# Kernel optimization log

Measured on AMD Instinct MI355X. Metric: run time of the kernel, lower is better.

The kernel has to match this reference:

```python
import jax, jax.numpy as jnp
import numpy as np

NUM_NODES = 32768  # B*N = 16*2048
NUM_REL = 10
NUM_BASES = 4
D = 256
E = 524288


def _rgcn_layer(x, src, dst, rel, basis, comp, root, bias):
    """Basis-decomposed relational GCN layer with per-relation mean aggregation.
    x: [N, Din], basis: [NB, Din, Dout], comp: [R, NB], root: [Din, Dout], bias: [Dout].
    """
    n = x.shape[0]
    # project all nodes through each basis once: [N, NB, Dout]
    xb = jnp.einsum('ni,bio->nbo', x, basis)
    coeff = comp[rel]  # [E, NB] per-edge basis coefficients
    # mean normalization per (destination node, relation) pair
    seg = rel * n + dst  # combined segment id, [E]
    cnt = jax.ops.segment_sum(jnp.ones(rel.shape[0], x.dtype), seg,
                              num_segments=NUM_REL * n)
    inv = jnp.where(cnt > 0, 1.0 / cnt, 0.0)[seg]  # [E]
    # per-edge message: sum_b coeff[e,b] * xb[src_e, b, :] (loop over small NB)
    msg = jnp.zeros((rel.shape[0], basis.shape[2]), x.dtype)
    for b in range(basis.shape[0]):
        msg = msg + coeff[:, b:b + 1] * xb[src, b]
    msg = msg * inv[:, None]
    agg = jax.ops.segment_sum(msg, dst, num_segments=n)  # [N, Dout]
    return agg + x @ root + bias


def setup_inputs() -> dict:
    key = jax.random.key(0)
    ks = jax.random.split(key, 16)
    p = lambda k, shp: (jax.random.normal(k, shp, jnp.float32) * 0.05)
    inp = {
        'x': jax.random.normal(ks[0], (16, 2048, D), jnp.float32),
        't': jax.random.randint(ks[1], (16,), 0, 1000),
        'obj_cond': jax.random.randint(ks[2], (16, 2048), 0, 160),
        'edge_cond': jax.random.randint(ks[3], (2, E), 0, NUM_NODES),
        'relation_cond': jax.random.randint(ks[4], (E,), 0, NUM_REL),
        # layer 0: 256 -> 256 (hidden)
        'basis0': p(ks[5], (NUM_BASES, D, D)),
        'comp0': p(ks[6], (NUM_REL, NUM_BASES)),
        'root0': p(ks[7], (D, D)),
        'bias0': p(ks[8], (D,)),
        # layer 1: 256 -> 256 (output)
        'basis1': p(ks[9], (NUM_BASES, D, D)),
        'comp1': p(ks[10], (NUM_REL, NUM_BASES)),
        'root1': p(ks[11], (D, D)),
        'bias1': p(ks[12], (D,)),
    }
    return inp


def reference(x, t, obj_cond, edge_cond, relation_cond,
              basis0, comp0, root0, bias0, basis1, comp1, root1, bias1):
    B, N, Dm = x.shape
    h = x.reshape(B * N, Dm)
    src, dst = edge_cond[0], edge_cond[1]
    h = _rgcn_layer(h, src, dst, relation_cond, basis0, comp0, root0, bias0)
    h = jax.nn.relu(h)  # hidden-layer activation (dropout disabled at eval)
    h = _rgcn_layer(h, src, dst, relation_cond, basis1, comp1, root1, bias1)
    return h.reshape(B, N, Dm)
```

## Files before the change

kernel.cpp:

```cpp
#include <hip/hip_runtime.h>
#include <stdint.h>

#define NNODES 32768
#define NREL 10
#define NBASES 4
#define DIM 256
#define NEDGE 524288
#define KW 1280
#define KBASE 1024

#define HB 2048
#define CB 8192
#define WB 80

typedef __attribute__((ext_vector_type(8))) short bf16x8;
typedef __attribute__((ext_vector_type(4))) float f32x4;
typedef __attribute__((ext_vector_type(2))) float f32x2;

__device__ __forceinline__ float bf2f(unsigned short u){
  union { unsigned int i; float f; } v; v.i = ((unsigned int)u) << 16; return v.f;
}
__device__ __forceinline__ float asf(unsigned int u){
  union { unsigned int i; float f; } v; v.i = u; return v.f;
}
__device__ __forceinline__ unsigned short f2bf(float f){
  union { float f; unsigned int i; } v; v.f = f;
  unsigned int x = v.i;
  unsigned int r = (x + 0x7FFFu + ((x >> 16) & 1u)) >> 16;
  return (unsigned short)r;
}
__device__ __forceinline__ void gll16(const void* g, void* l){
  __builtin_amdgcn_global_load_lds((const __attribute__((address_space(1))) void*)g,
                                   (__attribute__((address_space(3))) void*)l, 16, 0, 0);
}

__global__ __launch_bounds__(256) void mega_prep(
    const int* __restrict__ ec, const int* __restrict__ rel,
    int* __restrict__ cnt_rd,
    const float* __restrict__ x, unsigned short* __restrict__ Xh,
    const float* __restrict__ basis0, const float* __restrict__ root0,
    unsigned short* __restrict__ Wt0,
    const float* __restrict__ basis1, const float* __restrict__ root1,
    unsigned short* __restrict__ Wt1)
{
  __shared__ float tile[64][65];
  int bid = blockIdx.x;
  int t = threadIdx.x;
  if (bid < HB){
    int e = bid * 256 + t;
    int d = ec[NEDGE + e];
    int r = rel[e];
    atomicAdd(&cnt_rd[(r << 15) + d], 1);
  } else if (bid < HB + CB){
    int i = (bid - HB) * 256 + t;
    float4 v = ((const float4*)x)[i];
    ushort4 o; o.x = f2bf(v.x); o.y = f2bf(v.y); o.z = f2bf(v.z); o.w = f2bf(v.w);
    ((ushort4*)Xh)[i] = o;
  } else {
    int b = bid - HB - CB;
    int layer = b / WB; b %= WB;
    const float* basis = layer ? basis1 : basis0;
    const float* root  = layer ? root1  : root0;
    unsigned short* Wt = layer ? Wt1    : Wt0;
    int k0 = (b % 20) * 64;
    int n0 = (b / 20) * 64;
    int tn = t & 63, tk = t >> 6;
#pragma unroll
    for (int i = 0; i < 64; i += 4){
      int k = k0 + tk + i;
      float v = (k < KBASE) ? basis[(size_t)k * 256 + n0 + tn]
                            : root[(size_t)(k - KBASE) * 256 + n0 + tn];
      tile[tk + i][tn] = v;
    }
    __syncthreads();
#pragma unroll
    for (int i = 0; i < 64; i += 4){
      int n = n0 + tk + i;
      Wt[(size_t)n * KW + k0 + tn] = f2bf(tile[tn][tk + i]);
    }
  }
}

__global__ __launch_bounds__(1024) void scan1(const int* __restrict__ cnt_rd,
                                              int* __restrict__ offs, int* __restrict__ blksum)
{
  __shared__ int sh[1024];
  int tid = threadIdx.x; int gid = blockIdx.x * 1024 + tid;
  int v = 0;
#pragma unroll
  for (int r = 0; r < NREL; r++) v += cnt_rd[(r << 15) + gid];
  sh[tid] = v; __syncthreads();
  for (int off = 1; off < 1024; off <<= 1){
    int t = (tid >= off) ? sh[tid - off] : 0;
    __syncthreads(); sh[tid] += t; __syncthreads();
  }
  offs[gid] = sh[tid] - v;
  if (tid == 1023) blksum[blockIdx.x] = sh[1023];
}
__global__ __launch_bounds__(64) void scan2(int* __restrict__ blksum)
{
  __shared__ int sh[64];
  int tid = threadIdx.x;
  int v = (tid < NNODES / 1024) ? blksum[tid] : 0;
  sh[tid] = v; __syncthreads();
  for (int off = 1; off < 64; off <<= 1){
    int t = (tid >= off) ? sh[tid - off] : 0;
    __syncthreads(); sh[tid] += t; __syncthreads();
  }
  if (tid < NNODES / 1024) blksum[tid] = sh[tid] - v;
}
__global__ __launch_bounds__(1024) void scan3(int* __restrict__ offs, const int* __restrict__ blksum)
{
  int gid = blockIdx.x * 1024 + threadIdx.x;
  offs[gid] += blksum[blockIdx.x];
  if (gid == 0) offs[NNODES] = NEDGE;
}

__global__ void scatter_kernel(const int* __restrict__ ec, const int* __restrict__ rel,
                               const int* __restrict__ offs, int* __restrict__ cursor,
                               unsigned int* __restrict__ meta)
{
  int e = blockIdx.x * 256 + threadIdx.x;
  int s = ec[e];
  int d = ec[NEDGE + e];
  int r = rel[e];
  int p = offs[d] + atomicAdd(&cursor[d], 1);
  meta[p] = ((unsigned int)s << 4) | (unsigned int)r;
}

__global__ __launch_bounds__(256) void agg8(
    const unsigned short* __restrict__ Xin,
    const int* __restrict__ offs,
    const unsigned int* __restrict__ meta,
    const float* __restrict__ comp,
    const int* __restrict__ cnt_rd,
    unsigned short* __restrict__ z)
{
  __shared__ __attribute__((aligned(16))) float wtab[4][40];
  int t = threadIdx.x;
  int wv = t >> 6, lane = t & 63;
  int d = blockIdx.x * 4 + wv;
  if (lane < 40){
    int r = lane >> 2, b = lane & 3;
    int cnt = cnt_rd[(r << 15) + d];
    wtab[wv][lane] = (cnt > 0) ? comp[r * NBASES + b] / (float)cnt : 0.0f;
  }
  __syncthreads();

  const float4* wt4 = (const float4*)&wtab[wv][0];
  const char* Xb = (const char*)Xin;
  unsigned colb = (unsigned)(lane * 8);

  f32x2 acc[NBASES][2];
#pragma unroll
  for (int b = 0; b < NBASES; b++){ acc[b][0] = (f32x2){0.f,0.f}; acc[b][1] = (f32x2){0.f,0.f}; }

  int e0 = offs[d], e1 = offs[d + 1];
  int e = e0;

  for (; e + 7 < e1; e += 8){
    unsigned int m[8];
#pragma unroll
    for (int i = 0; i < 8; i++) m[i] = meta[e + i];
    uint2 v[8];
#pragma unroll
    for (int i = 0; i < 8; i++){
      unsigned off = ((m[i] & 0xFFFFFFF0u) << 5) + colb;
      v[i] = *(const uint2*)(Xb + off);
    }
#pragma unroll
    for (int i = 0; i < 8; i++){
      float4 w = wt4[m[i] & 15u];
      f32x2 f01, f23;
      f01.x = asf(v[i].x << 16); f01.y = asf(v[i].x & 0xffff0000u);
      f23.x = asf(v[i].y << 16); f23.y = asf(v[i].y & 0xffff0000u);
      acc[0][0] += (f32x2){w.x, w.x} * f01;  acc[0][1] += (f32x2){w.x, w.x} * f23;
      acc[1][0] += (f32x2){w.y, w.y} * f01;  acc[1][1] += (f32x2){w.y, w.y} * f23;
      acc[2][0] += (f32x2){w.z, w.z} * f01;  acc[2][1] += (f32x2){w.z, w.z} * f23;
      acc[3][0] += (f32x2){w.w, w.w} * f01;  acc[3][1] += (f32x2){w.w, w.w} * f23;
    }
  }

  for (; e < e1; e += 4){
    unsigned int m[4];
    float4 w[4];
#pragma unroll
    for (int i = 0; i < 4; i++){
      int ei = e + i;
      bool ok = ei < e1;
      m[i] = meta[ok ? ei : e1 - 1];
      float4 ww = wt4[m[i] & 15u];
      if (!ok){ ww.x = 0.f; ww.y = 0.f; ww.z = 0.f; ww.w = 0.f; }
      w[i] = ww;
    }
    uint2 v[4];
#pragma unroll
    for (int i = 0; i < 4; i++){
      unsigned off = ((m[i] & 0xFFFFFFF0u) << 5) + colb;
      v[i] = *(const uint2*)(Xb + off);
    }
#pragma unroll
    for (int i = 0; i < 4; i++){
      f32x2 f01, f23;
      f01.x = asf(v[i].x << 16); f01.y = asf(v[i].x & 0xffff0000u);
      f23.x = asf(v[i].y << 16); f23.y = asf(v[i].y & 0xffff0000u);
      acc[0][0] += (f32x2){w[i].x, w[i].x} * f01;  acc[0][1] += (f32x2){w[i].x, w[i].x} * f23;
      acc[1][0] += (f32x2){w[i].y, w[i].y} * f01;  acc[1][1] += (f32x2){w[i].y, w[i].y} * f23;
      acc[2][0] += (f32x2){w[i].z, w[i].z} * f01;  acc[2][1] += (f32x2){w[i].z, w[i].z} * f23;
      acc[3][0] += (f32x2){w[i].w, w[i].w} * f01;  acc[3][1] += (f32x2){w[i].w, w[i].w} * f23;
    }
  }

#pragma unroll
  for (int b = 0; b < NBASES; b++){
    ushort4 o;
    o.x = f2bf(acc[b][0].x); o.y = f2bf(acc[b][0].y);
    o.z = f2bf(acc[b][1].x); o.w = f2bf(acc[b][1].y);
    *(ushort4*)(z + (size_t)d * KBASE + b * 256 + lane * 4) = o;
  }
}

__global__ __launch_bounds__(256) void gemm6(
    const unsigned short* __restrict__ A0,
    const unsigned short* __restrict__ A1,
    const unsigned short* __restrict__ Wt,
    const float* __restrict__ bias,
    unsigned short* __restrict__ outh,
    float* __restrict__ outf,
    int mode)
{
  __shared__ __attribute__((aligned(16))) short As[2][64 * 32];
  __shared__ __attribute__((aligned(16))) short Bs[2][256 * 32];
  int tid  = threadIdx.x;
  int m0   = blockIdx.x * 64;
  int lane = tid & 63;
  int wn   = tid >> 6;
  int lq = lane >> 4, lr = lane & 15;

  f32x4 zero = {0.f, 0.f, 0.f, 0.f};
  f32x4 acc[4][4];
#pragma unroll
  for (int i = 0; i < 4; i++)
#pragma unroll
    for (int j = 0; j < 4; j++) acc[i][j] = zero;

  int arow = tid >> 2;
  int akc  = ((tid & 3) - (tid >> 3)) & 3;

#define STAGE(buf, kk) do {                                                   \
    const unsigned short* ga;                                                 \
    if ((kk) < KBASE) ga = A0 + (size_t)(m0 + arow) * KBASE + (kk) + akc * 8; \
    else              ga = A1 + (size_t)(m0 + arow) * 256 + ((kk) - KBASE) + akc * 8; \
    gll16(ga, &As[buf][tid * 8]);                                             \
    _Pragma("unroll")                                                         \
    for (int i_ = 0; i_ < 4; i_++){                                           \
      int gb_  = tid + i_ * 256;                                              \
      int row_ = gb_ >> 2;                                                    \
      int kc_  = ((gb_ & 3) - (gb_ >> 3)) & 3;                                \
      gll16(Wt + (size_t)row_ * KW + (kk) + kc_ * 8, &Bs[buf][gb_ * 8]);      \
    }                                                                         \
  } while (0)

#define COMPUTE(buf) do {                                                     \
    bf16x8 af[4], bfr[4];                                                     \
    _Pragma("unroll")                                                         \
    for (int i = 0; i < 4; i++){                                              \
      int row = i * 16 + lr;                                                  \
      af[i] = *(const bf16x8*)(&As[buf][row * 32 + (((lq + (row >> 1)) & 3) * 8)]); \
    }                                                                         \
    _Pragma("unroll")                                                         \
    for (int j = 0; j < 4; j++){                                              \
      int row = wn * 64 + j * 16 + lr;                                        \
      bfr[j] = *(const bf16x8*)(&Bs[buf][row * 32 + (((lq + (row >> 1)) & 3) * 8)]); \
    }                                                                         \
    _Pragma("unroll")                                                         \
    for (int i = 0; i < 4; i++)                                               \
      _Pragma("unroll")                                                       \
      for (int j = 0; j < 4; j++)                                             \
        acc[i][j] = __builtin_amdgcn_mfma_f32_16x16x32_bf16(af[i], bfr[j], acc[i][j], 0, 0, 0); \
  } while (0)

  const int NT = KW / 32;
  STAGE(0, 0);
  int cur = 0;

  for (int t = 0; t + 1 < NT; ++t){
    STAGE(cur ^ 1, (t + 1) * 32);
    __builtin_amdgcn_sched_barrier(0);
    asm volatile("s_waitcnt vmcnt(5)" ::: "memory");
    __builtin_amdgcn_s_barrier();
    __builtin_amdgcn_sched_barrier(0);
    COMPUTE(cur);
    __builtin_amdgcn_sched_barrier(0);
    __builtin_amdgcn_s_barrier();
    cur ^= 1;
  }
  __builtin_amdgcn_sched_barrier(0);
  asm volatile("s_waitcnt vmcnt(0)" ::: "memory");
  __builtin_amdgcn_s_barrier();
  __builtin_amdgcn_sched_barrier(0);
  COMPUTE(cur);
#undef STAGE
#undef COMPUTE

#pragma unroll
  for (int i = 0; i < 4; i++)
#pragma unroll
    for (int j = 0; j < 4; j++)
#pragma unroll
      for (int r = 0; r < 4; r++){
        int gm = m0 + i * 16 + lq * 4 + r;
        int gn = wn * 64 + j * 16 + lr;
        float v = acc[i][j][r] + bias[gn];
        size_t idx = (size_t)gm * 256 + gn;
        if (mode == 1) outh[idx] = f2bf(fmaxf(v, 0.f));
        else           outf[idx] = v;
      }
}

extern "C" void kernel_launch(void* const* d_in, const int* in_sizes, int n_in,
                              void* d_out, int out_size, void* d_ws, size_t ws_size,
                              hipStream_t stream)
{
  const float* x      = (const float*)d_in[0];
  const int*   ec     = (const int*)d_in[3];
  const int*   rel    = (const int*)d_in[4];
  const float* basis0 = (const float*)d_in[5];
  const float* comp0  = (const float*)d_in[6];
  const float* root0  = (const float*)d_in[7];
  const float* bias0  = (const float*)d_in[8];
  const float* basis1 = (const float*)d_in[9];
  const float* comp1  = (const float*)d_in[10];
  const float* root1  = (const float*)d_in[11];
  const float* bias1  = (const float*)d_in[12];

  char* p = (char*)d_ws;
  unsigned short* z   = (unsigned short*)p; p += (size_t)NNODES * KBASE * 2;
  unsigned short* Xh  = (unsigned short*)p; p += (size_t)NNODES * DIM * 2;
  unsigned short* h   = (unsigned short*)p; p += (size_t)NNODES * DIM * 2;
  unsigned short* Wt0 = (unsigned short*)p; p += (size_t)256 * KW * 2;
  unsigned short* Wt1 = (unsigned short*)p; p += (size_t)256 * KW * 2;
  unsigned int* meta  = (unsigned int*)p;   p += (size_t)NEDGE * 4;
  int* cnt_rd  = (int*)p;   p += (size_t)NREL * NNODES * 4;
  int* cursor  = (int*)p;   p += (size_t)NNODES * 4;
  int* offs    = (int*)p;   p += (size_t)(NNODES + 1) * 4;
  int* blksum  = (int*)p;   p += 1024;

  hipMemsetAsync(cnt_rd, 0, ((size_t)NREL * NNODES + (size_t)NNODES) * 4, stream);

  mega_prep<<<HB + CB + 2 * WB, 256, 0, stream>>>(
      ec, rel, cnt_rd, x, Xh, basis0, root0, Wt0, basis1, root1, Wt1);

  scan1<<<NNODES / 1024, 1024, 0, stream>>>(cnt_rd, offs, blksum);
  scan2<<<1, 64, 0, stream>>>(blksum);
  scan3<<<NNODES / 1024, 1024, 0, stream>>>(offs, blksum);
  scatter_kernel<<<NEDGE / 256, 256, 0, stream>>>(ec, rel, offs, cursor, meta);

  agg8<<<NNODES / 4, 256, 0, stream>>>(Xh, offs, meta, comp0, cnt_rd, z);
  gemm6<<<NNODES / 64, 256, 0, stream>>>(z, Xh, Wt0, bias0, h, nullptr, 1);

  agg8<<<NNODES / 4, 256, 0, stream>>>(h, offs, meta, comp1, cnt_rd, z);
  gemm6<<<NNODES / 64, 256, 0, stream>>>(z, h, Wt1, bias1, nullptr, (float*)d_out, 2);
}
```

Before: 330.8 us.

## Split GEMM N dimension across blocks and use triple-buffered LDS pipeline

The fused GEMM now tiles 64x128 per block instead of 64x256, doubling the grid and arranging the four waves 2x2. The LDS staging goes from double to triple buffering, keeping two tile loads in flight, with vmcnt waits adjusted to match. The intent is more blocks for occupancy and better hiding of global-load latency. The cost is that the A tile is now loaded twice, once per N half, and each wave issues fewer MFMAs per LDS read.

```diff
diff --git a/kernel.cpp b/kernel.cpp
--- a/kernel.cpp
+++ b/kernel.cpp
@@ -220,7 +220,7 @@
   }
 }
 
-__global__ __launch_bounds__(256) void gemm6(
+__global__ __launch_bounds__(256) void gemm7(
     const unsigned short* __restrict__ A0,
     const unsigned short* __restrict__ A1,
     const unsigned short* __restrict__ Wt,
@@ -229,18 +229,21 @@
     float* __restrict__ outf,
     int mode)
 {
-  __shared__ __attribute__((aligned(16))) short As[2][64 * 32];
-  __shared__ __attribute__((aligned(16))) short Bs[2][256 * 32];
+  __shared__ __attribute__((aligned(16))) short As[3][64 * 32];
+  __shared__ __attribute__((aligned(16))) short Bs[3][128 * 32];
   int tid  = threadIdx.x;
-  int m0   = blockIdx.x * 64;
+  int bid  = blockIdx.x;
+  int m0   = (bid >> 1) * 64;
+  int n0   = (bid & 1) * 128;
   int lane = tid & 63;
-  int wn   = tid >> 6;
+  int w    = tid >> 6;
+  int wm   = w >> 1, wn = w & 1;
   int lq = lane >> 4, lr = lane & 15;
 
   f32x4 zero = {0.f, 0.f, 0.f, 0.f};
-  f32x4 acc[4][4];
-#pragma unroll
-  for (int i = 0; i < 4; i++)
+  f32x4 acc[2][4];
+#pragma unroll
+  for (int i = 0; i < 2; i++)
 #pragma unroll
     for (int j = 0; j < 4; j++) acc[i][j] = zero;
 
@@ -253,19 +256,19 @@
     else              ga = A1 + (size_t)(m0 + arow) * 256 + ((kk) - KBASE) + akc * 8; \
     gll16(ga, &As[buf][tid * 8]);                                             \
     _Pragma("unroll")                                                         \
-    for (int i_ = 0; i_ < 4; i_++){                                           \
-      int gb_  = tid + i_ * 256;                                              \
-      int row_ = gb_ >> 2;                                                    \
+    for (int i_ = 0; i_ < 2; i_++){                                           \
+      int gb_  = tid + i_ * 256;                       \
+      int row_ = gb_ >> 2;                                        \
       int kc_  = ((gb_ & 3) - (gb_ >> 3)) & 3;                                \
-      gll16(Wt + (size_t)row_ * KW + (kk) + kc_ * 8, &Bs[buf][gb_ * 8]);      \
+      gll16(Wt + (size_t)(n0 + row_) * KW + (kk) + kc_ * 8, &Bs[buf][gb_ * 8]); \
     }                                                                         \
   } while (0)
 
 #define COMPUTE(buf) do {                                                     \
-    bf16x8 af[4], bfr[4];                                                     \
+    bf16x8 af[2], bfr[4];                                                     \
     _Pragma("unroll")                                                         \
-    for (int i = 0; i < 4; i++){                                              \
-      int row = i * 16 + lr;                                                  \
+    for (int i = 0; i < 2; i++){                                              \
+      int row = wm * 32 + i * 16 + lr;                                        \
       af[i] = *(const bf16x8*)(&As[buf][row * 32 + (((lq + (row >> 1)) & 3) * 8)]); \
     }                                                                         \
     _Pragma("unroll")                                                         \
@@ -274,7 +277,7 @@
       bfr[j] = *(const bf16x8*)(&Bs[buf][row * 32 + (((lq + (row >> 1)) & 3) * 8)]); \
     }                                                                         \
     _Pragma("unroll")                                                         \
-    for (int i = 0; i < 4; i++)                                               \
+    for (int i = 0; i < 2; i++)                                               \
       _Pragma("unroll")                                                       \
       for (int j = 0; j < 4; j++)                                             \
         acc[i][j] = __builtin_amdgcn_mfma_f32_16x16x32_bf16(af[i], bfr[j], acc[i][j], 0, 0, 0); \
@@ -282,35 +285,32 @@
 
   const int NT = KW / 32;
   STAGE(0, 0);
-  int cur = 0;
-
-  for (int t = 0; t + 1 < NT; ++t){
-    STAGE(cur ^ 1, (t + 1) * 32);
+  STAGE(1, 32);
+  STAGE(2, 64);
+
+  for (int t = 0; t < NT; ++t){
     __builtin_amdgcn_sched_barrier(0);
-    asm volatile("s_waitcnt vmcnt(5)" ::: "memory");
+    if (t < NT - 2)       asm volatile("s_waitcnt vmcnt(6)" ::: "memory");
+    else if (t == NT - 2) asm volatile("s_waitcnt vmcnt(3)" ::: "memory");
+    else                  asm volatile("s_waitcnt vmcnt(0)" ::: "memory");
     __builtin_amdgcn_s_barrier();
     __builtin_amdgcn_sched_barrier(0);
-    COMPUTE(cur);
+    COMPUTE(t % 3);
     __builtin_amdgcn_sched_barrier(0);
     __builtin_amdgcn_s_barrier();
-    cur ^= 1;
-  }
-  __builtin_amdgcn_sched_barrier(0);
-  asm volatile("s_waitcnt vmcnt(0)" ::: "memory");
-  __builtin_amdgcn_s_barrier();
-  __builtin_amdgcn_sched_barrier(0);
-  COMPUTE(cur);
+    if (t + 3 < NT) STAGE(t % 3, (t + 3) * 32);
+  }
 #undef STAGE
 #undef COMPUTE
 
 #pragma unroll
-  for (int i = 0; i < 4; i++)
+  for (int i = 0; i < 2; i++)
 #pragma unroll
     for (int j = 0; j < 4; j++)
 #pragma unroll
       for (int r = 0; r < 4; r++){
-        int gm = m0 + i * 16 + lq * 4 + r;
-        int gn = wn * 64 + j * 16 + lr;
+        int gm = m0 + wm * 32 + i * 16 + lq * 4 + r;
+        int gn = n0 + wn * 64 + j * 16 + lr;
         float v = acc[i][j][r] + bias[gn];
         size_t idx = (size_t)gm * 256 + gn;
         if (mode == 1) outh[idx] = f2bf(fmaxf(v, 0.f));
@@ -357,8 +357,8 @@
   scatter_kernel<<<NEDGE / 256, 256, 0, stream>>>(ec, rel, offs, cursor, meta);
 
   agg8<<<NNODES / 4, 256, 0, stream>>>(Xh, offs, meta, comp0, cnt_rd, z);
-  gemm6<<<NNODES / 64, 256, 0, stream>>>(z, Xh, Wt0, bias0, h, nullptr, 1);
+  gemm7<<<(NNODES / 64) * 2, 256, 0, stream>>>(z, Xh, Wt0, bias0, h, nullptr, 1);
 
   agg8<<<NNODES / 4, 256, 0, stream>>>(h, offs, meta, comp1, cnt_rd, z);
-  gemm6<<<NNODES / 64, 256, 0, stream>>>(z, h, Wt1, bias1, nullptr, (float*)d_out, 2);
-}
+  gemm7<<<(NNODES / 64) * 2, 256, 0, stream>>>(z, h, Wt1, bias1, nullptr, (float*)d_out, 2);
+}
```

Result: slower. 340.2 us (+2.8%).
